# Performance work log

Hardware: AMD Instinct MI355X
Metric: run time of the kernel (lower is better)

Reference implementation:

```python
import jax, jax.numpy as jnp
import numpy as np

D_STATE = 64
D_CONV = 4
DT_RANK = 16  # ceil(256/16)
LN_EPS = 1e-5


def _mamba_layer(x, ln_g, ln_b, in_w, conv_w, conv_b, xp_w, dt_w, dt_b, A_log, Dp, out_w):
    B, L, d_model = x.shape
    # LayerNorm (pre-norm)
    mu = x.mean(-1, keepdims=True)
    var = ((x - mu) ** 2).mean(-1, keepdims=True)
    xn = (x - mu) * jax.lax.rsqrt(var + LN_EPS) * ln_g + ln_b
    # in_proj -> split into x-branch and gate z
    xz = xn @ in_w.T                    # [B,L,2*d_inner]
    xm, z = jnp.split(xz, 2, axis=-1)   # each [B,L,d_inner]
    d_inner = xm.shape[-1]
    # causal depthwise conv1d (kernel D_CONV), then SiLU
    xp = jnp.pad(xm, ((0, 0), (D_CONV - 1, 0), (0, 0)))
    xc = conv_b + sum(xp[:, k:k + L, :] * conv_w[:, k] for k in range(D_CONV))
    xc = jax.nn.silu(xc)
    # input-dependent SSM params
    dbl = xc @ xp_w.T                   # [B,L,dt_rank+2*N]
    dt, Bm, Cm = jnp.split(dbl, [DT_RANK, DT_RANK + D_STATE], axis=-1)
    dt = jax.nn.softplus(dt @ dt_w.T + dt_b)   # [B,L,d_inner]
    A = -jnp.exp(A_log)                 # [d_inner, N]

    def step(h, inp):
        dt_t, B_t, C_t, u_t = inp       # [B,Di],[B,N],[B,N],[B,Di]
        dA = jnp.exp(dt_t[:, :, None] * A)                 # [B,Di,N]
        dBu = (dt_t * u_t)[:, :, None] * B_t[:, None, :]   # [B,Di,N]
        h = dA * h + dBu
        y = jnp.einsum('bdn,bn->bd', h, C_t)
        return h, y

    h0 = jnp.zeros((B, d_inner, D_STATE), x.dtype)
    _, ys = jax.lax.scan(
        step, h0,
        (dt.transpose(1, 0, 2), Bm.transpose(1, 0, 2), Cm.transpose(1, 0, 2), xc.transpose(1, 0, 2)))
    y = ys.transpose(1, 0, 2) + xc * Dp  # skip term D*u
    y = y * jax.nn.silu(z)               # gating
    out = y @ out_w.T                    # out_proj
    return out + x                       # residual


def reference(x, ln_g, ln_b, in_w, conv_w, conv_b, xp_w, dt_w, dt_b, A_log, Dp, out_w):
    depth = ln_g.shape[0]
    for i in range(depth):
        x = _mamba_layer(x, ln_g[i], ln_b[i], in_w[i], conv_w[i], conv_b[i],
                         xp_w[i], dt_w[i], dt_b[i], A_log[i], Dp[i], out_w[i])
    return x


def setup_inputs() -> dict:
    key = jax.random.key(0)
    ks = jax.random.split(key, 8)
    B, L, d_model, depth = 4, 1024, 256, 2
    d_inner = 2 * d_model
    x = jax.random.normal(ks[0], (B, L, d_model), jnp.float32)
    s = 0.02
    in_w = jax.random.normal(ks[1], (depth, 2 * d_inner, d_model), jnp.float32) * s
    conv_w = jax.random.normal(ks[2], (depth, d_inner, D_CONV), jnp.float32) * 0.3
    conv_b = jnp.zeros((depth, d_inner), jnp.float32)
    xp_w = jax.random.normal(ks[3], (depth, DT_RANK + 2 * D_STATE, d_inner), jnp.float32) * s
    dt_w = jax.random.normal(ks[4], (depth, d_inner, DT_RANK), jnp.float32) * 0.1
    # inverse-softplus of ~0.01 so dt starts small (mamba-style init)
    dt_b = jnp.full((depth, d_inner), float(np.log(np.expm1(0.01))), jnp.float32)
    # A = diag(1..N) per channel -> A_log = log(arange)
    A_log = jnp.broadcast_to(jnp.log(jnp.arange(1, D_STATE + 1, dtype=jnp.float32)),
                             (depth, d_inner, D_STATE))
    Dp = jnp.ones((depth, d_inner), jnp.float32)
    out_w = jax.random.normal(ks[5], (depth, d_model, d_inner), jnp.float32) * s
    ln_g = jnp.ones((depth, d_model), jnp.float32)
    ln_b = jnp.zeros((depth, d_model), jnp.float32)
    return {"x": x, "ln_g": ln_g, "ln_b": ln_b, "in_w": in_w, "conv_w": conv_w,
            "conv_b": conv_b, "xp_w": xp_w, "dt_w": dt_w, "dt_b": dt_b,
            "A_log": A_log, "Dp": Dp, "out_w": out_w}
```

## Files before the change

### kernel.cpp

```cpp
#include <hip/hip_runtime.h>
#include <math.h>

#define DI 512
#define DM 256
#define LSEQ 1024
#define BB 4
#define NST 64
#define ROWS (BB*LSEQ)
#define NC 16
#define CL 64

typedef __bf16 bf16x8 __attribute__((ext_vector_type(8)));
typedef __bf16 bf16x4 __attribute__((ext_vector_type(4)));
typedef float f32x4 __attribute__((ext_vector_type(4)));
typedef unsigned short u16;
typedef u16 u16x8 __attribute__((ext_vector_type(8)));

__device__ __forceinline__ float siluf(float x) { return x / (1.f + __expf(-x)); }
__device__ __forceinline__ float softplusf(float x) { return (x > 20.f) ? x : log1pf(__expf(x)); }
__device__ __forceinline__ float rlane(float v, int l) {
    return __int_as_float(__builtin_amdgcn_readlane(__float_as_int(v), l));
}
__device__ __forceinline__ float fexp2(float x) {
#if __has_builtin(__builtin_amdgcn_exp2f)
    return __builtin_amdgcn_exp2f(x);
#else
    return __expf(x * 0.69314718056f);
#endif
}

__device__ __forceinline__ float tree8(const float (&s)[8], int lane) {
    const bool b5 = (lane & 32) != 0;
    const bool b4 = (lane & 16) != 0;
    const bool b3 = (lane & 8) != 0;
    float r[4];
    #pragma unroll
    for (int i = 0; i < 4; ++i) {
        float u = b5 ? s[i+4] : s[i];
        float w = b5 ? s[i]   : s[i+4];
        r[i] = u + __shfl_xor(w, 32, 64);
    }
    float q[2];
    #pragma unroll
    for (int i = 0; i < 2; ++i) {
        float u = b4 ? r[i+2] : r[i];
        float w = b4 ? r[i]   : r[i+2];
        q[i] = u + __shfl_xor(w, 16, 64);
    }
    float u = b3 ? q[1] : q[0];
    float w = b3 ? q[0] : q[1];
    float p = u + __shfl_xor(w, 8, 64);
    p += __shfl_xor(p, 4, 64);
    p += __shfl_xor(p, 2, 64);
    p += __shfl_xor(p, 1, 64);
    return p;
}

__global__ __launch_bounds__(256) void f2bf(
    const float* __restrict__ in, __bf16* __restrict__ out, int n)
{
    int i = (blockIdx.x * 256 + threadIdx.x) * 4;
    if (i >= n) return;
    float4 v = *(const float4*)(in + i);
    bf16x4 o;
    o[0] = (__bf16)v.x; o[1] = (__bf16)v.y; o[2] = (__bf16)v.z; o[3] = (__bf16)v.w;
    *(bf16x4*)(out + i) = o;
}

__global__ __launch_bounds__(256) void ln_kernel(
    const float* __restrict__ x, const float* __restrict__ g,
    const float* __restrict__ b, __bf16* __restrict__ xn)
{
    int lane = threadIdx.x & 63;
    int row = blockIdx.x * 4 + (threadIdx.x >> 6);
    const float4* xr = (const float4*)(x + (size_t)row * DM);
    float4 v = xr[lane];
    float s = v.x + v.y + v.z + v.w;
    #pragma unroll
    for (int o = 32; o; o >>= 1) s += __shfl_xor(s, o, 64);
    float mu = s * (1.f / DM);
    float dx = v.x - mu, dy = v.y - mu, dz = v.z - mu, dw = v.w - mu;
    float q = dx*dx + dy*dy + dz*dz + dw*dw;
    #pragma unroll
    for (int o = 32; o; o >>= 1) q += __shfl_xor(q, o, 64);
    float inv = rsqrtf(q * (1.f / DM) + 1e-5f);
    float4 gv = ((const float4*)g)[lane];
    float4 bv = ((const float4*)b)[lane];
    bf16x4 o4;
    o4[0] = (__bf16)(dx * inv * gv.x + bv.x);
    o4[1] = (__bf16)(dy * inv * gv.y + bv.y);
    o4[2] = (__bf16)(dz * inv * gv.z + bv.z);
    o4[3] = (__bf16)(dw * inv * gv.w + bv.w);
    *(bf16x4*)(xn + (size_t)row * DM + lane * 4) = o4;
}

template<int KK>
__global__ __launch_bounds__(256) void gemm_mfma(
    const __bf16* __restrict__ A, const __bf16* __restrict__ W,
    float* __restrict__ C, __bf16* __restrict__ C2b,
    const float* __restrict__ res, int N, int mode)
{
    int wid = threadIdx.x >> 6, lane = threadIdx.x & 63;
    int wr = wid >> 1, wc = wid & 1;
    int bm = blockIdx.y * 64, bn = blockIdx.x * 64;
    int l15 = lane & 15, lk = (lane >> 4) * 8;
    const __bf16* Ap = A + (size_t)(bm + wr*32 + l15) * KK + lk;
    int wrow0 = bn + wc*32 + l15;
    int wrow1 = wrow0 + 16;
    if (wrow0 > N-1) wrow0 = N-1;
    if (wrow1 > N-1) wrow1 = N-1;
    const __bf16* Wp0 = W + (size_t)wrow0 * KK + lk;
    const __bf16* Wp1 = W + (size_t)wrow1 * KK + lk;
    f32x4 acc[2][2] = {};
    #pragma unroll 4
    for (int k0 = 0; k0 < KK; k0 += 32) {
        bf16x8 b0 = *(const bf16x8*)(Wp0 + k0);
        bf16x8 b1 = *(const bf16x8*)(Wp1 + k0);
        #pragma unroll
        for (int m = 0; m < 2; ++m) {
            bf16x8 a = *(const bf16x8*)(Ap + (size_t)m*16*KK + k0);
            acc[m][0] = __builtin_amdgcn_mfma_f32_16x16x32_bf16(a, b0, acc[m][0], 0, 0, 0);
            acc[m][1] = __builtin_amdgcn_mfma_f32_16x16x32_bf16(a, b1, acc[m][1], 0, 0, 0);
        }
    }
    int r4 = (lane >> 4) * 4;
    #pragma unroll
    for (int m = 0; m < 2; ++m) {
        int row = bm + wr*32 + m*16 + r4;
        #pragma unroll
        for (int n = 0; n < 2; ++n) {
            int col = bn + wc*32 + n*16 + l15;
            #pragma unroll
            for (int r = 0; r < 4; ++r) {
                float v = acc[m][n][r];
                int rr = row + r;
                if (mode == 0) {
                    if (col < N) C[(size_t)rr * N + col] = v;
                } else if (mode == 1) {
                    if (col < 512) C[(size_t)rr * 512 + col] = v;
                    else           C2b[(size_t)rr * 512 + col - 512] = (__bf16)v;
                } else {
                    C[(size_t)rr * N + col] = v + res[(size_t)rr * N + col];
                }
            }
        }
    }
}

__global__ __launch_bounds__(256) void gemm_dt(
    const float* __restrict__ A, int lda,
    const float* __restrict__ W,
    float* __restrict__ CT, const float* __restrict__ aux)
{
    __shared__ float As[16][68];
    __shared__ float Ws[16][68];
    const int bm = blockIdx.y * 64;
    const int bn = blockIdx.x * 64;
    const int tid = threadIdx.x;
    const int tx = tid & 15;
    const int ty = tid >> 4;
    const int lr = tid >> 2;
    const int lc = (tid & 3) << 2;
    float acc[4][4] = {};

    {
        float4 av = *(const float4*)(A + (size_t)(bm + lr) * lda + lc);
        float4 wv = *(const float4*)(W + (size_t)(bn + lr) * 16 + lc);
        As[lc+0][lr] = av.x; As[lc+1][lr] = av.y; As[lc+2][lr] = av.z; As[lc+3][lr] = av.w;
        Ws[lc+0][lr] = wv.x; Ws[lc+1][lr] = wv.y; Ws[lc+2][lr] = wv.z; Ws[lc+3][lr] = wv.w;
        __syncthreads();
        #pragma unroll
        for (int k = 0; k < 16; ++k) {
            float a[4], w[4];
            #pragma unroll
            for (int i = 0; i < 4; ++i) a[i] = As[k][ty*4 + i];
            #pragma unroll
            for (int j = 0; j < 4; ++j) w[j] = Ws[k][tx*4 + j];
            #pragma unroll
            for (int i = 0; i < 4; ++i)
                #pragma unroll
                for (int j = 0; j < 4; ++j)
                    acc[i][j] = fmaf(a[i], w[j], acc[i][j]);
        }
    }

    #pragma unroll
    for (int j = 0; j < 4; ++j) {
        int n = bn + tx*4 + j;
        float bia = aux[n];
        float4 v;
        v.x = softplusf(acc[0][j] + bia);
        v.y = softplusf(acc[1][j] + bia);
        v.z = softplusf(acc[2][j] + bia);
        v.w = softplusf(acc[3][j] + bia);
        *(float4*)(CT + (size_t)n * ROWS + bm + ty*4) = v;
    }
}

__global__ __launch_bounds__(256) void conv_silu_kernel(
    const float* __restrict__ xm, const float* __restrict__ cw,
    const float* __restrict__ cb, __bf16* __restrict__ xcb)
{
    int idx = blockIdx.x * 256 + threadIdx.x;
    int d = idx & (DI - 1);
    int row = idx >> 9;
    int t = row & (LSEQ - 1);
    float w0 = cw[d*4+0], w1 = cw[d*4+1], w2 = cw[d*4+2], w3 = cw[d*4+3];
    float acc = cb[d];
    const float* p = xm + (size_t)row * DI + d;
    if (t >= 3) {
        acc += p[-3*DI]*w0 + p[-2*DI]*w1 + p[-1*DI]*w2 + p[0]*w3;
    } else {
        if (t >= 2) acc += p[-2*DI]*w1;
        if (t >= 1) acc += p[-1*DI]*w2;
        acc += p[0]*w3;
    }
    xcb[idx] = (__bf16)siluf(acc);
}

__global__ __launch_bounds__(256) void transpose_bf(
    const u16* __restrict__ in, u16* __restrict__ out, int ldi, int ldo)
{
    __shared__ u16 tile[64][72];
    int r = threadIdx.x >> 2;
    int c0 = (threadIdx.x & 3) * 16;
    const u16* ip = in + (size_t)(blockIdx.y*64 + r) * ldi + blockIdx.x*64 + c0;
    *(u16x8*)&tile[r][c0]     = *(const u16x8*)(ip);
    *(u16x8*)&tile[r][c0 + 8] = *(const u16x8*)(ip + 8);
    __syncthreads();
    u16* op = out + (size_t)(blockIdx.x*64 + r) * ldo + blockIdx.y*64 + c0;
    u16x8 v0, v1;
    #pragma unroll
    for (int i = 0; i < 8; ++i) { v0[i] = tile[c0+i][r]; v1[i] = tile[c0+8+i][r]; }
    *(u16x8*)(op)     = v0;
    *(u16x8*)(op + 8) = v1;
}

__global__ __launch_bounds__(256) void scan_p1T(
    const float* __restrict__ dtT, const __bf16* __restrict__ xcT,
    const float* __restrict__ dbl, const float* __restrict__ A_log,
    float* __restrict__ Pe, float* __restrict__ He)
{
    int wid = (blockIdx.x * 256 + threadIdx.x) >> 6;
    int lane = threadIdx.x & 63;
    int c = wid & (NC - 1);
    int d = (wid >> 4) & (DI - 1);
    int b = wid >> 13;
    float An2 = -__expf(A_log[d * NST + lane]) * 1.44269504f;
    size_t row0 = (size_t)b * LSEQ + (size_t)c * CL;
    size_t tix = (size_t)d * ROWS + row0;
    float dtv = dtT[tix + lane];
    float uvf = (float)xcT[tix + lane];
    float duv = dtv * uvf;
    float Sdt = dtv;
    #pragma unroll
    for (int o = 32; o; o >>= 1) Sdt += __shfl_xor(Sdt, o, 64);
    const float* bp = dbl + row0 * 144 + 16 + lane;
    float H = 0.f;
    #pragma unroll
    for (int j = 0; j < 8; ++j) {
        #pragma unroll
        for (int q = 0; q < 8; ++q) {
            const int t = 8*j + q;
            float dA = fexp2(rlane(dtv, t) * An2);
            H = fmaf(dA, H, rlane(duv, t) * bp[q * 144]);
        }
        bp += 8 * 144;
    }
    size_t o = (size_t)wid * 64 + lane;
    Pe[o] = fexp2(An2 * Sdt);
    He[o] = H;
}

__global__ __launch_bounds__(256) void scan_carry(
    float* __restrict__ Pe, const float* __restrict__ He)
{
    int wid = (blockIdx.x * 256 + threadIdx.x) >> 6;
    int lane = threadIdx.x & 63;
    size_t base = (size_t)wid * NC * 64 + lane;
    float p[15], q[15];
    #pragma unroll
    for (int j = 0; j < 15; ++j) {
        p[j] = Pe[base + (size_t)j * 64];
        q[j] = He[base + (size_t)j * 64];
    }
    float h = 0.f;
    #pragma unroll
    for (int j = 0; j < 15; ++j) {
        h = fmaf(p[j], h, q[j]);
        Pe[base + (size_t)j * 64] = h;
    }
}

__global__ __launch_bounds__(256) void scan_p2T(
    const float* __restrict__ dtT, const __bf16* __restrict__ xcT,
    const __bf16* __restrict__ zT, const float* __restrict__ dbl,
    const float* __restrict__ A_log, const float* __restrict__ Dp,
    const float* __restrict__ Pe, __bf16* __restrict__ yT)
{
    __shared__ float Ys[4][64];
    int wid = (blockIdx.x * 256 + threadIdx.x) >> 6;
    int w = threadIdx.x >> 6;
    int lane = threadIdx.x & 63;
    int c = wid & (NC - 1);
    int d = (wid >> 4) & (DI - 1);
    int b = wid >> 13;
    float An2 = -__expf(A_log[d * NST + lane]) * 1.44269504f;
    size_t row0 = (size_t)b * LSEQ + (size_t)c * CL;
    size_t tix = (size_t)d * ROWS + row0;
    float dtv = dtT[tix + lane];
    float uvf = (float)xcT[tix + lane];
    float zvf = (float)zT[tix + lane];
    float duv = dtv * uvf;
    float gD  = uvf * Dp[d];
    float wz  = siluf(zvf);
    float h = (c == 0) ? 0.f : Pe[(size_t)(wid - 1) * 64 + lane];
    const float* bp = dbl + row0 * 144 + 16 + lane;
    const float* cp = dbl + row0 * 144 + 80 + lane;
    float yred[8];
    #pragma unroll
    for (int j = 0; j < 8; ++j) {
        float s[8];
        #pragma unroll
        for (int q = 0; q < 8; ++q) {
            const int t = 8*j + q;
            float dA = fexp2(rlane(dtv, t) * An2);
            h = fmaf(dA, h, rlane(duv, t) * bp[q * 144]);
            s[q] = h * cp[q * 144];
        }
        yred[j] = tree8(s, lane);
        bp += 8 * 144;
        cp += 8 * 144;
    }
    if ((lane & 7) == 0) {
        #pragma unroll
        for (int j = 0; j < 8; ++j) Ys[w][8*j + (lane >> 3)] = yred[j];
    }
    float y = (Ys[w][lane] + gD) * wz;
    yT[tix + lane] = (__bf16)y;
}

extern "C" void kernel_launch(void* const* d_in, const int* in_sizes, int n_in,
                              void* d_out, int out_size, void* d_ws, size_t ws_size,
                              hipStream_t stream)
{
    const float* x      = (const float*)d_in[0];
    const float* ln_g   = (const float*)d_in[1];
    const float* ln_b   = (const float*)d_in[2];
    const float* in_w   = (const float*)d_in[3];
    const float* conv_w = (const float*)d_in[4];
    const float* conv_b = (const float*)d_in[5];
    const float* xp_w   = (const float*)d_in[6];
    const float* dt_w   = (const float*)d_in[7];
    const float* dt_b   = (const float*)d_in[8];
    const float* A_log  = (const float*)d_in[9];
    const float* Dp     = (const float*)d_in[10];
    const float* out_w  = (const float*)d_in[11];
    float* out = (float*)d_out;

    char* ws = (char*)d_ws;
    const size_t MB = 1u << 20;
    float*  xm   = (float*)(ws + 0*MB);
    float*  Pe   = (float*)(ws + 0*MB);
    float*  dtT  = (float*)(ws + 8*MB);
    __bf16* xcbf = (__bf16*)(ws + 16*MB);
    __bf16* yTb  = (__bf16*)(ws + 16*MB);
    __bf16* xcT  = (__bf16*)(ws + 20*MB);
    __bf16* zbf  = (__bf16*)(ws + 24*MB);
    __bf16* ybf  = (__bf16*)(ws + 24*MB);
    __bf16* zT   = (__bf16*)(ws + 28*MB);
    float*  He   = (float*)(ws + 32*MB);
    float*  dblb = (float*)(ws + 40*MB);
    __bf16* xnb  = (__bf16*)(ws + 43*MB);
    __bf16* w_in  = (__bf16*)(ws + 45*MB);
    __bf16* w_xp  = (__bf16*)(ws + 46*MB);
    __bf16* w_out = (__bf16*)(ws + 46*MB + 512*1024);

    f2bf<<<512, 256, 0, stream>>>(in_w,  w_in,  2*1024*DM);
    f2bf<<<144, 256, 0, stream>>>(xp_w,  w_xp,  2*144*DI);
    f2bf<<<256, 256, 0, stream>>>(out_w, w_out, 2*DM*DI);

    for (int l = 0; l < 2; ++l) {
        const float* xin = (l == 0) ? x : out;
        ln_kernel<<<ROWS/4, 256, 0, stream>>>(xin, ln_g + l*DM, ln_b + l*DM, xnb);
        gemm_mfma<DM><<<dim3(1024/64, ROWS/64), 256, 0, stream>>>(
            xnb, w_in + (size_t)l*1024*DM, xm, zbf, nullptr, 1024, 1);
        conv_silu_kernel<<<(ROWS*DI)/256, 256, 0, stream>>>(
            xm, conv_w + (size_t)l*DI*4, conv_b + (size_t)l*DI, xcbf);
        gemm_mfma<DI><<<dim3(3, ROWS/64), 256, 0, stream>>>(
            xcbf, w_xp + (size_t)l*144*DI, dblb, nullptr, nullptr, 144, 0);
        transpose_bf<<<dim3(DI/64, ROWS/64), 256, 0, stream>>>(
            (const u16*)xcbf, (u16*)xcT, DI, ROWS);
        transpose_bf<<<dim3(DI/64, ROWS/64), 256, 0, stream>>>(
            (const u16*)zbf, (u16*)zT, DI, ROWS);
        gemm_dt<<<dim3(DI/64, ROWS/64), 256, 0, stream>>>(
            dblb, 144, dt_w + (size_t)l*DI*16, dtT, dt_b + (size_t)l*DI);
        scan_p1T<<<(BB*DI*NC)/4, 256, 0, stream>>>(
            dtT, xcT, dblb, A_log + (size_t)l*DI*NST, Pe, He);
        scan_carry<<<(BB*DI)/4, 256, 0, stream>>>(Pe, He);
        scan_p2T<<<(BB*DI*NC)/4, 256, 0, stream>>>(
            dtT, xcT, zT, dblb, A_log + (size_t)l*DI*NST, Dp + (size_t)l*DI,
            Pe, yTb);
        transpose_bf<<<dim3(ROWS/64, DI/64), 256, 0, stream>>>(
            (const u16*)yTb, (u16*)ybf, ROWS, DI);
        gemm_mfma<DI><<<dim3(DM/64, ROWS/64), 256, 0, stream>>>(
            ybf, w_out + (size_t)l*DM*DI, out, nullptr, xin, DM, 2);
    }
}
```

Measured before the change: 325.5 us.

## Fuse conv with transposes, inline chunk carry into scan, use DPP swizzles

Merges the causal conv+SiLU with the two bf16 transposes (xc and z) into one tiled kernel that stages rows in shared memory, which removes two launches and a round-trip of xc through global memory. It also drops the separate scan_carry kernel: each chunk in scan_p2T now recomputes its incoming state by folding all earlier chunk summaries. That adds redundant work that grows with the chunk index, up to 15 steps. The tree reduction switches from shfl_xor to permlane32_swap and ds_swizzle to make the cross-lane traffic cheaper.

```diff
diff --git a/kernel.cpp b/kernel.cpp
--- a/kernel.cpp
+++ b/kernel.cpp
@@ -15,6 +15,7 @@
 typedef float f32x4 __attribute__((ext_vector_type(4)));
 typedef unsigned short u16;
 typedef u16 u16x8 __attribute__((ext_vector_type(8)));
+typedef int i32x2 __attribute__((ext_vector_type(2)));
 
 __device__ __forceinline__ float siluf(float x) { return x / (1.f + __expf(-x)); }
 __device__ __forceinline__ float softplusf(float x) { return (x > 20.f) ? x : log1pf(__expf(x)); }
@@ -28,31 +29,44 @@
     return __expf(x * 0.69314718056f);
 #endif
 }
+template<int PAT>
+__device__ __forceinline__ float fswz(float v) {
+    return __int_as_float(__builtin_amdgcn_ds_swizzle(__float_as_int(v), PAT));
+}
 
 __device__ __forceinline__ float tree8(const float (&s)[8], int lane) {
-    const bool b5 = (lane & 32) != 0;
     const bool b4 = (lane & 16) != 0;
     const bool b3 = (lane & 8) != 0;
     float r[4];
+#if __has_builtin(__builtin_amdgcn_permlane32_swap)
+    #pragma unroll
+    for (int i = 0; i < 4; ++i) {
+        i32x2 pr = __builtin_amdgcn_permlane32_swap(
+            __float_as_int(s[i]), __float_as_int(s[i+4]), false, false);
+        r[i] = __int_as_float(pr[0]) + __int_as_float(pr[1]);
+    }
+#else
+    const bool b5 = (lane & 32) != 0;
     #pragma unroll
     for (int i = 0; i < 4; ++i) {
         float u = b5 ? s[i+4] : s[i];
         float w = b5 ? s[i]   : s[i+4];
         r[i] = u + __shfl_xor(w, 32, 64);
     }
+#endif
     float q[2];
     #pragma unroll
     for (int i = 0; i < 2; ++i) {
         float u = b4 ? r[i+2] : r[i];
         float w = b4 ? r[i]   : r[i+2];
-        q[i] = u + __shfl_xor(w, 16, 64);
+        q[i] = u + fswz<0x401F>(w);
     }
     float u = b3 ? q[1] : q[0];
     float w = b3 ? q[0] : q[1];
-    float p = u + __shfl_xor(w, 8, 64);
-    p += __shfl_xor(p, 4, 64);
-    p += __shfl_xor(p, 2, 64);
-    p += __shfl_xor(p, 1, 64);
+    float p = u + fswz<0x201F>(w);
+    p += fswz<0x101F>(p);
+    p += fswz<0x081F>(p);
+    p += fswz<0x041F>(p);
     return p;
 }
 
@@ -162,7 +176,6 @@
     const int lr = tid >> 2;
     const int lc = (tid & 3) << 2;
     float acc[4][4] = {};
-
     {
         float4 av = *(const float4*)(A + (size_t)(bm + lr) * lda + lc);
         float4 wv = *(const float4*)(W + (size_t)(bn + lr) * 16 + lc);
@@ -183,7 +196,6 @@
                     acc[i][j] = fmaf(a[i], w[j], acc[i][j]);
         }
     }
-
     #pragma unroll
     for (int j = 0; j < 4; ++j) {
         int n = bn + tx*4 + j;
@@ -197,25 +209,71 @@
     }
 }
 
-__global__ __launch_bounds__(256) void conv_silu_kernel(
+__global__ __launch_bounds__(256) void conv_tr_kernel(
     const float* __restrict__ xm, const float* __restrict__ cw,
-    const float* __restrict__ cb, __bf16* __restrict__ xcb)
-{
-    int idx = blockIdx.x * 256 + threadIdx.x;
-    int d = idx & (DI - 1);
-    int row = idx >> 9;
-    int t = row & (LSEQ - 1);
-    float w0 = cw[d*4+0], w1 = cw[d*4+1], w2 = cw[d*4+2], w3 = cw[d*4+3];
-    float acc = cb[d];
-    const float* p = xm + (size_t)row * DI + d;
-    if (t >= 3) {
-        acc += p[-3*DI]*w0 + p[-2*DI]*w1 + p[-1*DI]*w2 + p[0]*w3;
-    } else {
-        if (t >= 2) acc += p[-2*DI]*w1;
-        if (t >= 1) acc += p[-1*DI]*w2;
-        acc += p[0]*w3;
-    }
-    xcb[idx] = (__bf16)siluf(acc);
+    const float* __restrict__ cb, const u16* __restrict__ zin,
+    __bf16* __restrict__ xcb, u16* __restrict__ xcT, u16* __restrict__ zT)
+{
+    __shared__ float xs[67][66];
+    __shared__ u16 Tc[64][72];
+    __shared__ u16 Tz[64][72];
+    const int tid = threadIdx.x;
+    const int row0 = blockIdx.y * 64;
+    const int d0 = blockIdx.x * 64;
+    #pragma unroll
+    for (int it = 0; it < 5; ++it) {
+        int f4 = it * 256 + tid;
+        if (f4 < 67 * 16) {
+            int rr = f4 >> 4;
+            int cc = (f4 & 15) * 4;
+            int g = row0 - 3 + rr;
+            float4 v = make_float4(0.f, 0.f, 0.f, 0.f);
+            if (g >= 0 && (g >> 10) == (row0 >> 10))
+                v = *(const float4*)(xm + (size_t)g * DI + d0 + cc);
+            *(float4*)&xs[rr][cc] = v;
+        }
+    }
+    const int r = tid >> 2;
+    const int c0 = (tid & 3) * 16;
+    {
+        const u16* zp = zin + (size_t)(row0 + r) * DI + d0 + c0;
+        *(u16x8*)&Tz[r][c0]     = *(const u16x8*)(zp);
+        *(u16x8*)&Tz[r][c0 + 8] = *(const u16x8*)(zp + 8);
+    }
+    __syncthreads();
+    {
+        bf16x8 v0, v1;
+        #pragma unroll
+        for (int j = 0; j < 16; ++j) {
+            int d = d0 + c0 + j;
+            float acc = cb[d]
+                + xs[r+0][c0+j] * cw[d*4+0]
+                + xs[r+1][c0+j] * cw[d*4+1]
+                + xs[r+2][c0+j] * cw[d*4+2]
+                + xs[r+3][c0+j] * cw[d*4+3];
+            __bf16 o = (__bf16)siluf(acc);
+            if (j < 8) v0[j] = o; else v1[j-8] = o;
+            Tc[r][c0+j] = *(const u16*)&o;
+        }
+        __bf16* op = xcb + (size_t)(row0 + r) * DI + d0 + c0;
+        *(bf16x8*)(op)     = v0;
+        *(bf16x8*)(op + 8) = v1;
+    }
+    __syncthreads();
+    {
+        u16x8 a0, a1, b0, b1;
+        #pragma unroll
+        for (int i = 0; i < 8; ++i) {
+            a0[i] = Tc[c0+i][r];   a1[i] = Tc[c0+8+i][r];
+            b0[i] = Tz[c0+i][r];   b1[i] = Tz[c0+8+i][r];
+        }
+        u16* oc = xcT + (size_t)(d0 + r) * ROWS + row0 + c0;
+        u16* oz = zT  + (size_t)(d0 + r) * ROWS + row0 + c0;
+        *(u16x8*)(oc)     = a0;
+        *(u16x8*)(oc + 8) = a1;
+        *(u16x8*)(oz)     = b0;
+        *(u16x8*)(oz + 8) = b1;
+    }
 }
 
 __global__ __launch_bounds__(256) void transpose_bf(
@@ -272,31 +330,12 @@
     He[o] = H;
 }
 
-__global__ __launch_bounds__(256) void scan_carry(
-    float* __restrict__ Pe, const float* __restrict__ He)
-{
-    int wid = (blockIdx.x * 256 + threadIdx.x) >> 6;
-    int lane = threadIdx.x & 63;
-    size_t base = (size_t)wid * NC * 64 + lane;
-    float p[15], q[15];
-    #pragma unroll
-    for (int j = 0; j < 15; ++j) {
-        p[j] = Pe[base + (size_t)j * 64];
-        q[j] = He[base + (size_t)j * 64];
-    }
-    float h = 0.f;
-    #pragma unroll
-    for (int j = 0; j < 15; ++j) {
-        h = fmaf(p[j], h, q[j]);
-        Pe[base + (size_t)j * 64] = h;
-    }
-}
-
 __global__ __launch_bounds__(256) void scan_p2T(
     const float* __restrict__ dtT, const __bf16* __restrict__ xcT,
     const __bf16* __restrict__ zT, const float* __restrict__ dbl,
     const float* __restrict__ A_log, const float* __restrict__ Dp,
-    const float* __restrict__ Pe, __bf16* __restrict__ yT)
+    const float* __restrict__ Pe, const float* __restrict__ He,
+    __bf16* __restrict__ yT)
 {
     __shared__ float Ys[4][64];
     int wid = (blockIdx.x * 256 + threadIdx.x) >> 6;
@@ -314,7 +353,14 @@
     float duv = dtv * uvf;
     float gD  = uvf * Dp[d];
     float wz  = siluf(zvf);
-    float h = (c == 0) ? 0.f : Pe[(size_t)(wid - 1) * 64 + lane];
+    float h = 0.f;
+    {
+        int cbase = wid - c;
+        for (int j = 0; j < c; ++j) {
+            size_t o = (size_t)(cbase + j) * 64 + lane;
+            h = fmaf(Pe[o], h, He[o]);
+        }
+    }
     const float* bp = dbl + row0 * 144 + 16 + lane;
     const float* cp = dbl + row0 * 144 + 80 + lane;
     float yred[8];
@@ -385,22 +431,18 @@
         ln_kernel<<<ROWS/4, 256, 0, stream>>>(xin, ln_g + l*DM, ln_b + l*DM, xnb);
         gemm_mfma<DM><<<dim3(1024/64, ROWS/64), 256, 0, stream>>>(
             xnb, w_in + (size_t)l*1024*DM, xm, zbf, nullptr, 1024, 1);
-        conv_silu_kernel<<<(ROWS*DI)/256, 256, 0, stream>>>(
-            xm, conv_w + (size_t)l*DI*4, conv_b + (size_t)l*DI, xcbf);
+        conv_tr_kernel<<<dim3(DI/64, ROWS/64), 256, 0, stream>>>(
+            xm, conv_w + (size_t)l*DI*4, conv_b + (size_t)l*DI,
+            (const u16*)zbf, xcbf, (u16*)xcT, (u16*)zT);
         gemm_mfma<DI><<<dim3(3, ROWS/64), 256, 0, stream>>>(
             xcbf, w_xp + (size_t)l*144*DI, dblb, nullptr, nullptr, 144, 0);
-        transpose_bf<<<dim3(DI/64, ROWS/64), 256, 0, stream>>>(
-            (const u16*)xcbf, (u16*)xcT, DI, ROWS);
-        transpose_bf<<<dim3(DI/64, ROWS/64), 256, 0, stream>>>(
-            (const u16*)zbf, (u16*)zT, DI, ROWS);
         gemm_dt<<<dim3(DI/64, ROWS/64), 256, 0, stream>>>(
             dblb, 144, dt_w + (size_t)l*DI*16, dtT, dt_b + (size_t)l*DI);
         scan_p1T<<<(BB*DI*NC)/4, 256, 0, stream>>>(
             dtT, xcT, dblb, A_log + (size_t)l*DI*NST, Pe, He);
-        scan_carry<<<(BB*DI)/4, 256, 0, stream>>>(Pe, He);
         scan_p2T<<<(BB*DI*NC)/4, 256, 0, stream>>>(
             dtT, xcT, zT, dblb, A_log + (size_t)l*DI*NST, Dp + (size_t)l*DI,
-            Pe, yTb);
+            Pe, He, yTb);
         transpose_bf<<<dim3(ROWS/64, DI/64), 256, 0, stream>>>(
             (const u16*)yTb, (u16*)ybf, ROWS, DI);
         gemm_mfma<DI><<<dim3(DM/64, ROWS/64), 256, 0, stream>>>(
```

New measurement: 314.6 us. 1.03x faster.
